# Kernel optimization log

Hardware: AMD Instinct MI355X
Metric: run time of the kernel (lower is better)

The kernel has to match this reference:

```python
import jax, jax.numpy as jnp
import numpy as np

B, H, W, C = 32, 512, 512, 3
OUT_H, OUT_W = 224, 224


def setup_inputs() -> dict:
    key = jax.random.key(0)
    k1, k2 = jax.random.split(key)
    images = jax.random.uniform(k1, (B, H, W, C), dtype=jnp.float32)
    identity = jnp.array([[1.0, 0.0, 0.0], [0.0, 1.0, 0.0]], dtype=jnp.float32)
    matrices = identity[None] + 0.05 * jax.random.normal(k2, (B, 2, 3), dtype=jnp.float32)
    return {"images": images, "matrices": matrices}


def _affine_warp(image, M):
    # image: (H, W, C); M: (2, 3) mapping output pixel (y, x, 1) -> source (y, x).
    h, w, _ = image.shape
    dt = image.dtype
    ys, xs = jnp.meshgrid(jnp.arange(h, dtype=dt), jnp.arange(w, dtype=dt), indexing="ij")
    src_y = M[0, 0] * ys + M[0, 1] * xs + M[0, 2]
    src_x = M[1, 0] * ys + M[1, 1] * xs + M[1, 2]
    y0 = jnp.floor(src_y)
    x0 = jnp.floor(src_x)
    wy = (src_y - y0)[..., None]
    wx = (src_x - x0)[..., None]
    y0i = y0.astype(jnp.int32)
    x0i = x0.astype(jnp.int32)

    def gather(yi, xi):
        valid = (yi >= 0) & (yi < h) & (xi >= 0) & (xi < w)
        yc = jnp.clip(yi, 0, h - 1)
        xc = jnp.clip(xi, 0, w - 1)
        return image[yc, xc] * valid[..., None].astype(dt)  # zero fill outside

    v00 = gather(y0i, x0i)
    v01 = gather(y0i, x0i + 1)
    v10 = gather(y0i + 1, x0i)
    v11 = gather(y0i + 1, x0i + 1)
    top = v00 * (1.0 - wx) + v01 * wx
    bot = v10 * (1.0 - wx) + v11 * wx
    return top * (1.0 - wy) + bot * wy


def reference(images, matrices):
    # batch_transform: per-sample affine warp (bilinear sampling, zero padding)
    warped = jax.vmap(_affine_warp)(images, matrices)  # (B, H, W, C)
    # batch_resize: bilinear resize to the layer's target shape
    b, _, _, c = warped.shape
    return jax.image.resize(warped, (b, OUT_H, OUT_W, c), method="bilinear")
```

## Files before the change

### kernel.cpp

```cpp
#include <hip/hip_runtime.h>
#include <math.h>

constexpr int B  = 32;
constexpr int H  = 512;
constexpr int W  = 512;
constexpr int C  = 3;
constexpr int OH = 224;
constexpr int OW = 224;

constexpr int TILE = 16;
constexpr int WIN  = 40;
constexpr int NT   = OH / TILE;
constexpr int NB   = B * NT * NT;
constexpr int THREADS = 320;

__global__ __launch_bounds__(THREADS) void warp_resize_tiled(const float* __restrict__ img,
                                                             const float* __restrict__ mats,
                                                             float* __restrict__ out) {
    __shared__ float sW[WIN][WIN * 3];
    __shared__ float sV[TILE][WIN * 3];

    int bid = (int)blockIdx.x;
    bid = (bid & 7) * (NB / 8) + (bid >> 3);

    const int b   = bid / (NT * NT);
    const int rm  = bid % (NT * NT);
    const int ty  = rm / NT;
    const int tx  = rm % NT;
    const int tid = (int)threadIdx.x;

    const float* Mp = mats + b * 6;
    const float m00 = Mp[0], m01 = Mp[1], m02 = Mp[2];
    const float m10 = Mp[3], m11 = Mp[4], m12 = Mp[5];

    const float s     = 512.0f / 224.0f;
    const float invks = 224.0f / 512.0f;

    const int oy_base = ty * TILE;
    const int ox_base = tx * TILE;
    const int jy0 = (int)ceilf((oy_base + 0.5f) * s - 0.5f - s);
    const int jx0 = (int)ceilf((ox_base + 0.5f) * s - 0.5f - s);

    const float* imgb = img + (size_t)b * H * W * C;

    const float y_lo = (float)jy0, y_hi = (float)(jy0 + WIN - 1);
    const float x_lo = (float)jx0, x_hi = (float)(jx0 + WIN - 1);
    float cy00 = m00 * y_lo + m01 * x_lo + m02;
    float cy01 = m00 * y_lo + m01 * x_hi + m02;
    float cy10 = m00 * y_hi + m01 * x_lo + m02;
    float cy11 = m00 * y_hi + m01 * x_hi + m02;
    float cx00 = m10 * y_lo + m11 * x_lo + m12;
    float cx01 = m10 * y_lo + m11 * x_hi + m12;
    float cx10 = m10 * y_hi + m11 * x_lo + m12;
    float cx11 = m10 * y_hi + m11 * x_hi + m12;
    const float miny = fminf(fminf(cy00, cy01), fminf(cy10, cy11));
    const float maxy = fmaxf(fmaxf(cy00, cy01), fmaxf(cy10, cy11));
    const float minx = fminf(fminf(cx00, cx01), fminf(cx10, cx11));
    const float maxx = fmaxf(fmaxf(cx00, cx01), fmaxf(cx10, cx11));
    const bool interior = (miny >= 0.01f) && (maxy <= 510.9f) &&
                          (minx >= 0.01f) && (maxx <= 510.9f);

    {
        const int c  = tid % WIN;
        int       r  = tid / WIN;
        const float xf = (float)(jx0 + c);
        const float cY = m01 * xf + m02;
        const float cX = m11 * xf + m12;

        if (interior) {
#pragma unroll
            for (int it = 0; it < 5; ++it) {
                const float yf = (float)(jy0 + r);
                const float src_y = m00 * yf + cY;
                const float src_x = m10 * yf + cX;
                const float fy0 = floorf(src_y);
                const float fx0 = floorf(src_x);
                const float fy  = src_y - fy0;
                const float fx  = src_x - fx0;
                const int off = ((int)fy0 * W + (int)fx0) * 3;
                const float* p0 = imgb + off;
                const float* p1 = p0 + W * 3;
                const float a0 = p0[0], a1 = p0[1], a2 = p0[2];
                const float a3 = p0[3], a4 = p0[4], a5 = p0[5];
                const float b0 = p1[0], b1 = p1[1], b2 = p1[2];
                const float b3 = p1[3], b4 = p1[4], b5 = p1[5];
                const float w00 = (1.0f - fy) * (1.0f - fx);
                const float w01 = (1.0f - fy) * fx;
                const float w10 = fy * (1.0f - fx);
                const float w11 = fy * fx;
                sW[r][c * 3 + 0] = a0 * w00 + a3 * w01 + b0 * w10 + b3 * w11;
                sW[r][c * 3 + 1] = a1 * w00 + a4 * w01 + b1 * w10 + b4 * w11;
                sW[r][c * 3 + 2] = a2 * w00 + a5 * w01 + b2 * w10 + b5 * w11;
                r += 8;
            }
        } else {
#pragma unroll
            for (int it = 0; it < 5; ++it) {
                const float yf = (float)(jy0 + r);
                const float src_y = m00 * yf + cY;
                const float src_x = m10 * yf + cX;
                const float fy0 = floorf(src_y);
                const float fx0 = floorf(src_x);
                const float fy  = src_y - fy0;
                const float fx  = src_x - fx0;
                const int iy0 = (int)fy0;
                const int ix0 = (int)fx0;
                float v[4][3];
#pragma unroll
                for (int t = 0; t < 4; ++t) {
                    const int yi = iy0 + (t >> 1);
                    const int xi = ix0 + (t & 1);
                    if (yi >= 0 && yi < H && xi >= 0 && xi < W) {
                        const float* p = imgb + (yi * W + xi) * 3;
                        v[t][0] = p[0]; v[t][1] = p[1]; v[t][2] = p[2];
                    } else {
                        v[t][0] = 0.0f; v[t][1] = 0.0f; v[t][2] = 0.0f;
                    }
                }
                const float w00 = (1.0f - fy) * (1.0f - fx);
                const float w01 = (1.0f - fy) * fx;
                const float w10 = fy * (1.0f - fx);
                const float w11 = fy * fx;
                sW[r][c * 3 + 0] = v[0][0] * w00 + v[1][0] * w01 + v[2][0] * w10 + v[3][0] * w11;
                sW[r][c * 3 + 1] = v[0][1] * w00 + v[1][1] * w01 + v[2][1] * w10 + v[3][1] * w11;
                sW[r][c * 3 + 2] = v[0][2] * w00 + v[1][2] * w01 + v[2][2] * w10 + v[3][2] * w11;
                r += 8;
            }
        }
    }
    __syncthreads();

    {
        const int c = tid % WIN;
        int       r = tid / WIN;
#pragma unroll
        for (int it = 0; it < 2; ++it) {
            const int oy = oy_base + r;
            const float sfy = (oy + 0.5f) * s - 0.5f;
            const int j0 = (int)ceilf(sfy - s);
            float wk[5];
            float sum = 0.0f;
#pragma unroll
            for (int k = 0; k < 5; ++k) {
                const int jy = j0 + k;
                float wv = 1.0f - fabsf(sfy - (float)jy) * invks;
                wv = (jy >= 0 && jy < H) ? fmaxf(wv, 0.0f) : 0.0f;
                wk[k] = wv; sum += wv;
            }
            const float inv = 1.0f / sum;
            float a0 = 0.0f, a1 = 0.0f, a2 = 0.0f;
#pragma unroll
            for (int k = 0; k < 5; ++k) {
                const int rr = j0 + k - jy0;
                const float wv = wk[k];
                a0 += wv * sW[rr][c * 3 + 0];
                a1 += wv * sW[rr][c * 3 + 1];
                a2 += wv * sW[rr][c * 3 + 2];
            }
            sV[r][c * 3 + 0] = a0 * inv;
            sV[r][c * 3 + 1] = a1 * inv;
            sV[r][c * 3 + 2] = a2 * inv;
            r += 8;
        }
    }
    __syncthreads();

    if (tid < TILE * TILE) {
        const int oxl = tid % TILE;
        const int oyl = tid / TILE;
        const int ox  = ox_base + oxl;
        const int oy  = oy_base + oyl;
        const float sfx = (ox + 0.5f) * s - 0.5f;
        const int j0 = (int)ceilf(sfx - s);
        float wk[5];
        float sum = 0.0f;
#pragma unroll
        for (int k = 0; k < 5; ++k) {
            const int jx = j0 + k;
            float wv = 1.0f - fabsf(sfx - (float)jx) * invks;
            wv = (jx >= 0 && jx < W) ? fmaxf(wv, 0.0f) : 0.0f;
            wk[k] = wv; sum += wv;
        }
        const float inv = 1.0f / sum;
        float a0 = 0.0f, a1 = 0.0f, a2 = 0.0f;
#pragma unroll
        for (int k = 0; k < 5; ++k) {
            const int cc = j0 + k - jx0;
            const float wv = wk[k];
            a0 += wv * sV[oyl][cc * 3 + 0];
            a1 += wv * sV[oyl][cc * 3 + 1];
            a2 += wv * sV[oyl][cc * 3 + 2];
        }
        float* o = out + (((size_t)b * OH + oy) * OW + ox) * 3;
        o[0] = a0 * inv;
        o[1] = a1 * inv;
        o[2] = a2 * inv;
    }
}

extern "C" void kernel_launch(void* const* d_in, const int* in_sizes, int n_in,
                              void* d_out, int out_size, void* d_ws, size_t ws_size,
                              hipStream_t stream) {
    const float* img  = (const float*)d_in[0];
    const float* mats = (const float*)d_in[1];
    float*       out  = (float*)d_out;

    hipLaunchKernelGGL(warp_resize_tiled, dim3(NB), dim3(THREADS), 0, stream, img, mats, out);
}
```

Baseline: 162.6 us.

## Store warped window in bf16 planar shared memory and use 256-thread blocks

Cuts the block size from 320 to 256 threads so the final output stage uses every thread, and asks for 8 blocks per CU through launch bounds. The warped intermediate window becomes channel-planar bf16 instead of interleaved fp32, which shrinks shared memory to allow higher occupancy and changes the bank access pattern. Work loops become strided over all elements instead of fixed unrolled iterations. Rounding the intermediate to bf16 costs accuracy and may push results past the tolerance.

```diff
diff --git a/kernel.cpp b/kernel.cpp
--- a/kernel.cpp
+++ b/kernel.cpp
@@ -1,10 +1,10 @@
 #include <hip/hip_runtime.h>
+#include <hip/hip_bf16.h>
 #include <math.h>
 
 constexpr int B  = 32;
 constexpr int H  = 512;
 constexpr int W  = 512;
-constexpr int C  = 3;
 constexpr int OH = 224;
 constexpr int OW = 224;
 
@@ -12,13 +12,13 @@
 constexpr int WIN  = 40;
 constexpr int NT   = OH / TILE;
 constexpr int NB   = B * NT * NT;
-constexpr int THREADS = 320;
+constexpr int THREADS = 256;
 
-__global__ __launch_bounds__(THREADS) void warp_resize_tiled(const float* __restrict__ img,
-                                                             const float* __restrict__ mats,
-                                                             float* __restrict__ out) {
-    __shared__ float sW[WIN][WIN * 3];
-    __shared__ float sV[TILE][WIN * 3];
+__global__ __launch_bounds__(THREADS, 8) void warp_resize_tiled(const float* __restrict__ img,
+                                                                const float* __restrict__ mats,
+                                                                float* __restrict__ out) {
+    __shared__ __hip_bfloat16 sWp[3][WIN][WIN];
+    __shared__ float          sV[TILE][WIN * 3];
 
     int bid = (int)blockIdx.x;
     bid = (bid & 7) * (NB / 8) + (bid >> 3);
@@ -41,18 +41,18 @@
     const int jy0 = (int)ceilf((oy_base + 0.5f) * s - 0.5f - s);
     const int jx0 = (int)ceilf((ox_base + 0.5f) * s - 0.5f - s);
 
-    const float* imgb = img + (size_t)b * H * W * C;
+    const float* imgb = img + (size_t)b * H * W * 3;
 
     const float y_lo = (float)jy0, y_hi = (float)(jy0 + WIN - 1);
     const float x_lo = (float)jx0, x_hi = (float)(jx0 + WIN - 1);
-    float cy00 = m00 * y_lo + m01 * x_lo + m02;
-    float cy01 = m00 * y_lo + m01 * x_hi + m02;
-    float cy10 = m00 * y_hi + m01 * x_lo + m02;
-    float cy11 = m00 * y_hi + m01 * x_hi + m02;
-    float cx00 = m10 * y_lo + m11 * x_lo + m12;
-    float cx01 = m10 * y_lo + m11 * x_hi + m12;
-    float cx10 = m10 * y_hi + m11 * x_lo + m12;
-    float cx11 = m10 * y_hi + m11 * x_hi + m12;
+    const float cy00 = m00 * y_lo + m01 * x_lo + m02;
+    const float cy01 = m00 * y_lo + m01 * x_hi + m02;
+    const float cy10 = m00 * y_hi + m01 * x_lo + m02;
+    const float cy11 = m00 * y_hi + m01 * x_hi + m02;
+    const float cx00 = m10 * y_lo + m11 * x_lo + m12;
+    const float cx01 = m10 * y_lo + m11 * x_hi + m12;
+    const float cx10 = m10 * y_hi + m11 * x_lo + m12;
+    const float cx11 = m10 * y_hi + m11 * x_hi + m12;
     const float miny = fminf(fminf(cy00, cy01), fminf(cy10, cy11));
     const float maxy = fmaxf(fmaxf(cy00, cy01), fmaxf(cy10, cy11));
     const float minx = fminf(fminf(cx00, cx01), fminf(cx10, cx11));
@@ -60,112 +60,102 @@
     const bool interior = (miny >= 0.01f) && (maxy <= 510.9f) &&
                           (minx >= 0.01f) && (maxx <= 510.9f);
 
-    {
-        const int c  = tid % WIN;
-        int       r  = tid / WIN;
-        const float xf = (float)(jx0 + c);
-        const float cY = m01 * xf + m02;
-        const float cX = m11 * xf + m12;
-
-        if (interior) {
+    if (interior) {
+        for (int e = tid; e < WIN * WIN; e += THREADS) {
+            const int r = e / WIN;
+            const int c = e - r * WIN;
+            const float yf = (float)(jy0 + r);
+            const float xf = (float)(jx0 + c);
+            const float src_y = m00 * yf + m01 * xf + m02;
+            const float src_x = m10 * yf + m11 * xf + m12;
+            const float fy0 = floorf(src_y);
+            const float fx0 = floorf(src_x);
+            const float fy  = src_y - fy0;
+            const float fx  = src_x - fx0;
+            const int off = ((int)fy0 * W + (int)fx0) * 3;
+            const float* p0 = imgb + off;
+            const float* p1 = p0 + W * 3;
+            const float a0 = p0[0], a1 = p0[1], a2 = p0[2];
+            const float a3 = p0[3], a4 = p0[4], a5 = p0[5];
+            const float b0 = p1[0], b1 = p1[1], b2 = p1[2];
+            const float b3 = p1[3], b4 = p1[4], b5 = p1[5];
+            const float w00 = (1.0f - fy) * (1.0f - fx);
+            const float w01 = (1.0f - fy) * fx;
+            const float w10 = fy * (1.0f - fx);
+            const float w11 = fy * fx;
+            sWp[0][r][c] = __float2bfloat16(a0 * w00 + a3 * w01 + b0 * w10 + b3 * w11);
+            sWp[1][r][c] = __float2bfloat16(a1 * w00 + a4 * w01 + b1 * w10 + b4 * w11);
+            sWp[2][r][c] = __float2bfloat16(a2 * w00 + a5 * w01 + b2 * w10 + b5 * w11);
+        }
+    } else {
+        for (int e = tid; e < WIN * WIN; e += THREADS) {
+            const int r = e / WIN;
+            const int c = e - r * WIN;
+            const float yf = (float)(jy0 + r);
+            const float xf = (float)(jx0 + c);
+            const float src_y = m00 * yf + m01 * xf + m02;
+            const float src_x = m10 * yf + m11 * xf + m12;
+            const float fy0 = floorf(src_y);
+            const float fx0 = floorf(src_x);
+            const float fy  = src_y - fy0;
+            const float fx  = src_x - fx0;
+            const int iy0 = (int)fy0;
+            const int ix0 = (int)fx0;
+            float v[4][3];
 #pragma unroll
-            for (int it = 0; it < 5; ++it) {
-                const float yf = (float)(jy0 + r);
-                const float src_y = m00 * yf + cY;
-                const float src_x = m10 * yf + cX;
-                const float fy0 = floorf(src_y);
-                const float fx0 = floorf(src_x);
-                const float fy  = src_y - fy0;
-                const float fx  = src_x - fx0;
-                const int off = ((int)fy0 * W + (int)fx0) * 3;
-                const float* p0 = imgb + off;
-                const float* p1 = p0 + W * 3;
-                const float a0 = p0[0], a1 = p0[1], a2 = p0[2];
-                const float a3 = p0[3], a4 = p0[4], a5 = p0[5];
-                const float b0 = p1[0], b1 = p1[1], b2 = p1[2];
-                const float b3 = p1[3], b4 = p1[4], b5 = p1[5];
-                const float w00 = (1.0f - fy) * (1.0f - fx);
-                const float w01 = (1.0f - fy) * fx;
-                const float w10 = fy * (1.0f - fx);
-                const float w11 = fy * fx;
-                sW[r][c * 3 + 0] = a0 * w00 + a3 * w01 + b0 * w10 + b3 * w11;
-                sW[r][c * 3 + 1] = a1 * w00 + a4 * w01 + b1 * w10 + b4 * w11;
-                sW[r][c * 3 + 2] = a2 * w00 + a5 * w01 + b2 * w10 + b5 * w11;
-                r += 8;
+            for (int t = 0; t < 4; ++t) {
+                const int yi = iy0 + (t >> 1);
+                const int xi = ix0 + (t & 1);
+                if (yi >= 0 && yi < H && xi >= 0 && xi < W) {
+                    const float* p = imgb + (yi * W + xi) * 3;
+                    v[t][0] = p[0]; v[t][1] = p[1]; v[t][2] = p[2];
+                } else {
+                    v[t][0] = 0.0f; v[t][1] = 0.0f; v[t][2] = 0.0f;
+                }
             }
-        } else {
-#pragma unroll
-            for (int it = 0; it < 5; ++it) {
-                const float yf = (float)(jy0 + r);
-                const float src_y = m00 * yf + cY;
-                const float src_x = m10 * yf + cX;
-                const float fy0 = floorf(src_y);
-                const float fx0 = floorf(src_x);
-                const float fy  = src_y - fy0;
-                const float fx  = src_x - fx0;
-                const int iy0 = (int)fy0;
-                const int ix0 = (int)fx0;
-                float v[4][3];
-#pragma unroll
-                for (int t = 0; t < 4; ++t) {
-                    const int yi = iy0 + (t >> 1);
-                    const int xi = ix0 + (t & 1);
-                    if (yi >= 0 && yi < H && xi >= 0 && xi < W) {
-                        const float* p = imgb + (yi * W + xi) * 3;
-                        v[t][0] = p[0]; v[t][1] = p[1]; v[t][2] = p[2];
-                    } else {
-                        v[t][0] = 0.0f; v[t][1] = 0.0f; v[t][2] = 0.0f;
-                    }
-                }
-                const float w00 = (1.0f - fy) * (1.0f - fx);
-                const float w01 = (1.0f - fy) * fx;
-                const float w10 = fy * (1.0f - fx);
-                const float w11 = fy * fx;
-                sW[r][c * 3 + 0] = v[0][0] * w00 + v[1][0] * w01 + v[2][0] * w10 + v[3][0] * w11;
-                sW[r][c * 3 + 1] = v[0][1] * w00 + v[1][1] * w01 + v[2][1] * w10 + v[3][1] * w11;
-                sW[r][c * 3 + 2] = v[0][2] * w00 + v[1][2] * w01 + v[2][2] * w10 + v[3][2] * w11;
-                r += 8;
-            }
+            const float w00 = (1.0f - fy) * (1.0f - fx);
+            const float w01 = (1.0f - fy) * fx;
+            const float w10 = fy * (1.0f - fx);
+            const float w11 = fy * fx;
+            sWp[0][r][c] = __float2bfloat16(v[0][0] * w00 + v[1][0] * w01 + v[2][0] * w10 + v[3][0] * w11);
+            sWp[1][r][c] = __float2bfloat16(v[0][1] * w00 + v[1][1] * w01 + v[2][1] * w10 + v[3][1] * w11);
+            sWp[2][r][c] = __float2bfloat16(v[0][2] * w00 + v[1][2] * w01 + v[2][2] * w10 + v[3][2] * w11);
         }
     }
     __syncthreads();
 
-    {
-        const int c = tid % WIN;
-        int       r = tid / WIN;
+    for (int e = tid; e < TILE * WIN; e += THREADS) {
+        const int r = e / WIN;
+        const int c = e - r * WIN;
+        const int oy = oy_base + r;
+        const float sfy = (oy + 0.5f) * s - 0.5f;
+        const int j0 = (int)ceilf(sfy - s);
+        float wk[5];
+        float sum = 0.0f;
 #pragma unroll
-        for (int it = 0; it < 2; ++it) {
-            const int oy = oy_base + r;
-            const float sfy = (oy + 0.5f) * s - 0.5f;
-            const int j0 = (int)ceilf(sfy - s);
-            float wk[5];
-            float sum = 0.0f;
+        for (int k = 0; k < 5; ++k) {
+            const int jy = j0 + k;
+            float wv = 1.0f - fabsf(sfy - (float)jy) * invks;
+            wv = (jy >= 0 && jy < H) ? fmaxf(wv, 0.0f) : 0.0f;
+            wk[k] = wv; sum += wv;
+        }
+        const float inv = 1.0f / sum;
+        float a0 = 0.0f, a1 = 0.0f, a2 = 0.0f;
 #pragma unroll
-            for (int k = 0; k < 5; ++k) {
-                const int jy = j0 + k;
-                float wv = 1.0f - fabsf(sfy - (float)jy) * invks;
-                wv = (jy >= 0 && jy < H) ? fmaxf(wv, 0.0f) : 0.0f;
-                wk[k] = wv; sum += wv;
-            }
-            const float inv = 1.0f / sum;
-            float a0 = 0.0f, a1 = 0.0f, a2 = 0.0f;
-#pragma unroll
-            for (int k = 0; k < 5; ++k) {
-                const int rr = j0 + k - jy0;
-                const float wv = wk[k];
-                a0 += wv * sW[rr][c * 3 + 0];
-                a1 += wv * sW[rr][c * 3 + 1];
-                a2 += wv * sW[rr][c * 3 + 2];
-            }
-            sV[r][c * 3 + 0] = a0 * inv;
-            sV[r][c * 3 + 1] = a1 * inv;
-            sV[r][c * 3 + 2] = a2 * inv;
-            r += 8;
+        for (int k = 0; k < 5; ++k) {
+            const int rr = j0 + k - jy0;
+            const float wv = wk[k];
+            a0 += wv * __bfloat162float(sWp[0][rr][c]);
+            a1 += wv * __bfloat162float(sWp[1][rr][c]);
+            a2 += wv * __bfloat162float(sWp[2][rr][c]);
         }
+        sV[r][c * 3 + 0] = a0 * inv;
+        sV[r][c * 3 + 1] = a1 * inv;
+        sV[r][c * 3 + 2] = a2 * inv;
     }
     __syncthreads();
 
-    if (tid < TILE * TILE) {
+    {
         const int oxl = tid % TILE;
         const int oyl = tid / TILE;
         const int ox  = ox_base + oxl;
```

Result: no change. 161.1 us (-0.9%).
